# Kernel optimization log

Hardware: AMD Instinct MI355X
Metric: run time of the kernel (lower is better)

The kernel has to match this reference:

```python
import jax, jax.numpy as jnp
import numpy as np

E, D, H = 8, 512, 2048  # num_experts, features, features*mlp_ratio
B, S = 4, 512


def _lecun(key, shape):
    fan_in = shape[-2] if len(shape) >= 2 else shape[0]
    return jax.random.normal(key, shape, dtype=jnp.float32) / jnp.sqrt(jnp.float32(fan_in))


def setup_inputs() -> dict:
    key = jax.random.key(0)
    ks = jax.random.split(key, 8)
    return {
        'x_real': jax.random.normal(ks[0], (B, S, D), dtype=jnp.float32),
        'x_imag': jax.random.normal(ks[1], (B, S, D), dtype=jnp.float32),
        # gating Dense over concat([amp, phase]) -> in_features = 2*D
        'gate_W': _lecun(ks[2], (2 * D, E)),
        'gate_b': jnp.zeros((E,), jnp.float32),
        # per-expert ComplexLinear 1: D -> H
        'W1r': _lecun(ks[3], (E, D, H)),
        'W1i': _lecun(ks[4], (E, D, H)),
        'b1r': jnp.zeros((E, H), jnp.float32),
        'b1i': jnp.zeros((E, H), jnp.float32),
        # per-expert ComplexModReLU bias
        'mod_b': jnp.zeros((E, H), jnp.float32),
        # per-expert ComplexLinear 2: H -> D
        'W2r': _lecun(ks[5], (E, H, D)),
        'W2i': _lecun(ks[6], (E, H, D)),
        'b2r': jnp.zeros((E, D), jnp.float32),
        'b2i': jnp.zeros((E, D), jnp.float32),
    }


def reference(x_real, x_imag, gate_W, gate_b, W1r, W1i, b1r, b1i, mod_b, W2r, W2i, b2r, b2i):
    eps = 1e-10
    # --- gating: scores over [|z|, angle(z)] ---
    amp = jnp.sqrt(x_real ** 2 + x_imag ** 2)            # |z|, [B,S,D]
    phase = jnp.arctan2(x_imag, x_real)                  # angle(z)
    routing_input = jnp.concatenate([amp, phase], axis=-1)  # [B,S,2D]
    scores = routing_input @ gate_W + gate_b             # [B,S,E]
    probs = jax.nn.softmax(scores, axis=-1)
    idx = jnp.argmax(probs, axis=-1)                     # [B,S] top-1 expert

    # --- all experts dense (faithful to reference): complex linear 1 ---
    # (Wr + iWi)(xr + ixi) : hr = xr Wr - xi Wi ; hi = xr Wi + xi Wr
    h_r = (jnp.einsum('bsd,edh->ebsh', x_real, W1r)
           - jnp.einsum('bsd,edh->ebsh', x_imag, W1i)) + b1r[:, None, None, :]
    h_i = (jnp.einsum('bsd,edh->ebsh', x_real, W1i)
           + jnp.einsum('bsd,edh->ebsh', x_imag, W1r)) + b1i[:, None, None, :]

    # --- ComplexModReLU: relu(|z|+b) * z / (|z|+eps), |z| = sqrt(r^2+i^2+eps) ---
    a = jnp.sqrt(h_r ** 2 + h_i ** 2 + eps)              # [E,B,S,H]
    scale = jax.nn.relu(a + mod_b[:, None, None, :]) / (a + eps)
    h_r = h_r * scale
    h_i = h_i * scale

    # --- complex linear 2 ---
    o_r = (jnp.einsum('ebsh,ehd->ebsd', h_r, W2r)
           - jnp.einsum('ebsh,ehd->ebsd', h_i, W2i)) + b2r[:, None, None, :]
    o_i = (jnp.einsum('ebsh,ehd->ebsd', h_r, W2i)
           + jnp.einsum('ebsh,ehd->ebsd', h_i, W2r)) + b2i[:, None, None, :]

    # --- mask + weight (top-1): out = sum_e out_e * probs[...,e] * (argmax==e) ---
    e_ids = jnp.arange(probs.shape[-1])
    w = jnp.transpose(probs, (2, 0, 1)) * (idx[None, :, :] == e_ids[:, None, None])  # [E,B,S]
    out_r = jnp.einsum('ebs,ebsd->bsd', w, o_r)
    out_i = jnp.einsum('ebs,ebsd->bsd', w, o_i)
    return (out_r, out_i)
```

## Files before the change

kernel.cpp:

```cpp
#include <hip/hip_runtime.h>
#include <math.h>

#define NE 8
#define ND 512
#define NH 2048
#define NT 2048

typedef __attribute__((ext_vector_type(8))) short short8;
typedef __attribute__((ext_vector_type(4))) float f32x4;

#define GLL(g, d) __builtin_amdgcn_global_load_lds( \
    (const __attribute__((address_space(1))) void*)(g), \
    (__attribute__((address_space(3))) void*)(d), 16, 0, 0)

__device__ __forceinline__ unsigned short f2bf(float x) {
    unsigned int u = __builtin_bit_cast(unsigned int, x);
    u += 0x7FFFu + ((u >> 16) & 1u);
    return (unsigned short)(u >> 16);
}

__device__ __forceinline__ short8 lds8(const unsigned short* p) {
    return *(const short8*)p;
}

__global__ __launch_bounds__(256) void gate_kernel(
    const float* __restrict__ xr, const float* __restrict__ xi,
    const float* __restrict__ gW, const float* __restrict__ gb,
    float* __restrict__ gate_w,
    int* __restrict__ counts, int* __restrict__ tok_list)
{
    int t = blockIdx.x;
    int tid = threadIdx.x;
    const float* xrt = xr + (size_t)t * ND;
    const float* xit = xi + (size_t)t * ND;

    float acc[NE] = {0,0,0,0,0,0,0,0};
    for (int r = tid; r < 2 * ND; r += 256) {
        int d = r & (ND - 1);
        float a = xrt[d], b = xit[d];
        float v = (r < ND) ? sqrtf(a * a + b * b) : atan2f(b, a);
        const float4* g = (const float4*)(gW + (size_t)r * NE);
        float4 g0 = g[0], g1 = g[1];
        acc[0] += v * g0.x; acc[1] += v * g0.y; acc[2] += v * g0.z; acc[3] += v * g0.w;
        acc[4] += v * g1.x; acc[5] += v * g1.y; acc[6] += v * g1.z; acc[7] += v * g1.w;
    }
    #pragma unroll
    for (int e = 0; e < NE; e++) {
        for (int off = 32; off > 0; off >>= 1)
            acc[e] += __shfl_down(acc[e], off, 64);
    }
    __shared__ float part[4][NE];
    int wave = tid >> 6, lane = tid & 63;
    if (lane == 0) {
        #pragma unroll
        for (int e = 0; e < NE; e++) part[wave][e] = acc[e];
    }
    __syncthreads();
    if (tid == 0) {
        float s[NE];
        #pragma unroll
        for (int e = 0; e < NE; e++)
            s[e] = part[0][e] + part[1][e] + part[2][e] + part[3][e] + gb[e];
        int amax = 0; float m = s[0];
        #pragma unroll
        for (int e = 1; e < NE; e++) if (s[e] > m) { m = s[e]; amax = e; }
        float denom = 0.f;
        #pragma unroll
        for (int e = 0; e < NE; e++) denom += expf(s[e] - m);
        gate_w[t] = 1.0f / denom;
        int pos = atomicAdd(&counts[amax], 1);
        tok_list[amax * NT + pos] = t;
    }
}

__global__ __launch_bounds__(256) void convx_kernel(
    const float* __restrict__ xr, const float* __restrict__ xi,
    unsigned short* __restrict__ obr, unsigned short* __restrict__ obi)
{
    int i = blockIdx.x * 256 + threadIdx.x;
    float4 vr = ((const float4*)xr)[i];
    float4 vi = ((const float4*)xi)[i];
    ((ushort4*)obr)[i] = make_ushort4(f2bf(vr.x), f2bf(vr.y), f2bf(vr.z), f2bf(vr.w));
    ((ushort4*)obi)[i] = make_ushort4(f2bf(vi.x), f2bf(vi.y), f2bf(vi.z), f2bf(vi.w));
}

__global__ __launch_bounds__(256) void transw_kernel(
    const float* __restrict__ s0, unsigned short* __restrict__ d0,
    const float* __restrict__ s1, unsigned short* __restrict__ d1,
    int R, int C)
{
    __shared__ float tile[64][65];
    int e = blockIdx.z;
    int c0 = blockIdx.x * 64, r0 = blockIdx.y * 64;
    size_t off = (size_t)e * R * C;
    int tid = threadIdx.x;
    #pragma unroll
    for (int p = 0; p < 2; ++p) {
        const float* src = (p ? s1 : s0) + off;
        unsigned short* dst = (p ? d1 : d0) + off;
        if (p) __syncthreads();
        for (int i = 0; i < 16; ++i) {
            int idx = tid + i * 256;
            int r = idx >> 6, c = idx & 63;
            tile[r][c] = src[(size_t)(r0 + r) * C + c0 + c];
        }
        __syncthreads();
        #pragma unroll
        for (int i = 0; i < 4; ++i) {
            int c = i * 16 + (tid >> 4);
            int r4 = (tid & 15) * 4;
            ushort4 v = make_ushort4(f2bf(tile[r4][c]), f2bf(tile[r4 + 1][c]),
                                     f2bf(tile[r4 + 2][c]), f2bf(tile[r4 + 3][c]));
            *(ushort4*)&dst[(size_t)(c0 + c) * R + r0 + r4] = v;
        }
    }
}


#define STAGE_(SA_R, SA_I, SB_R, SB_I, ko) do {  \
    GLL(gAr0 + (ko), SA_R + (w * 16) * 64);      \
    GLL(gAi0 + (ko), SA_I + (w * 16) * 64);      \
    GLL(gAr1 + (ko), SA_R + (w * 16 + 8) * 64);  \
    GLL(gAi1 + (ko), SA_I + (w * 16 + 8) * 64);  \
    GLL(gBr0 + (ko), SB_R + (w * 16) * 64);      \
    GLL(gBr1 + (ko), SB_R + (w * 16 + 8) * 64);  \
    GLL(gBi0 + (ko), SB_I + (w * 16) * 64);      \
    GLL(gBi1 + (ko), SB_I + (w * 16 + 8) * 64);  \
} while (0)

#define COMPUTE_(SA_R, SA_I, SB_R, SB_I) do {                                          \
    _Pragma("unroll")                                                                  \
    for (int ks = 0; ks < 2; ++ks) {                                                   \
        int pa = ((ks * 4 + quad) ^ (l15 & 7)) * 8;                                    \
        short8 br  = lds8(SB_R + (w * 16 + l15) * 64 + pa);                            \
        short8 bi2 = lds8(SB_I + (w * 16 + l15) * 64 + pa);                            \
        _Pragma("unroll")                                                              \
        for (int m = 0; m < 4; ++m) {                                                  \
            short8 ar  = lds8(SA_R + (m * 16 + l15) * 64 + pa);                        \
            short8 ai2 = lds8(SA_I + (m * 16 + l15) * 64 + pa);                        \
            aRR[m] = __builtin_amdgcn_mfma_f32_16x16x32_bf16(ar,  br,  aRR[m], 0, 0, 0); \
            aII[m] = __builtin_amdgcn_mfma_f32_16x16x32_bf16(ai2, bi2, aII[m], 0, 0, 0); \
            aRI[m] = __builtin_amdgcn_mfma_f32_16x16x32_bf16(ar,  bi2, aRI[m], 0, 0, 0); \
            aIR[m] = __builtin_amdgcn_mfma_f32_16x16x32_bf16(ai2, br,  aIR[m], 0, 0, 0); \
        }                                                                              \
    }                                                                                  \
} while (0)

#define VMW8  asm volatile("s_waitcnt vmcnt(8)" ::: "memory")
#define VMW0  asm volatile("s_waitcnt vmcnt(0)" ::: "memory")
#define BARX do {                            \
    __builtin_amdgcn_sched_barrier(0);       \
    __builtin_amdgcn_s_barrier();            \
    __builtin_amdgcn_sched_barrier(0);       \
} while (0)

#define MOE_LDS_DECL                                                        \
    __shared__ alignas(16) unsigned short sAr0[4096], sAi0[4096];           \
    __shared__ alignas(16) unsigned short sBr0[4096], sBi0[4096];           \
    __shared__ alignas(16) unsigned short sAr1[4096], sAi1[4096];           \
    __shared__ alignas(16) unsigned short sBr1[4096], sBi1[4096];

#define PIPE_LOOP(NK) do {                                                  \
    STAGE_(sAr0, sAi0, sBr0, sBi0, 0);                                      \
    VMW0; BARX;                                                             \
    _Pragma("unroll 1")                                                     \
    for (int kt = 0; kt < (NK); kt += 2) {                                  \
        if (kt + 1 < (NK)) { STAGE_(sAr1, sAi1, sBr1, sBi1, (kt + 1) * 64); VMW8; } \
        else VMW0;                                                          \
        BARX;                                                               \
        COMPUTE_(sAr0, sAi0, sBr0, sBi0);                                   \
        BARX;                                                               \
        if (kt + 2 < (NK)) { STAGE_(sAr0, sAi0, sBr0, sBi0, (kt + 2) * 64); VMW8; } \
        else VMW0;                                                          \
        BARX;                                                               \
        COMPUTE_(sAr1, sAi1, sBr1, sBi1);                                   \
        BARX;                                                               \
    }                                                                       \
} while (0)

__global__ __launch_bounds__(256, 2) void moe1_kernel(
    const unsigned short* __restrict__ xbr, const unsigned short* __restrict__ xbi,
    const unsigned short* __restrict__ w1tr, const unsigned short* __restrict__ w1ti,
    const float* __restrict__ b1r, const float* __restrict__ b1i,
    const float* __restrict__ mod_b,
    const int* __restrict__ counts, const int* __restrict__ tok_list,
    unsigned short* __restrict__ hr, unsigned short* __restrict__ hi)
{
    int e = blockIdx.z;
    int n = counts[e];
    int mbase = blockIdx.y * 64;
    if (mbase >= n) return;
    int n0 = blockIdx.x * 64;
    int tid = threadIdx.x;
    int w = tid >> 6, l = tid & 63;
    int l15 = l & 15, quad = l >> 4;

    MOE_LDS_DECL

    const int* tl = tok_list + e * NT;
    int swz = (((l & 7) ^ ((l >> 3) & 7)) * 8);
    int ia0 = mbase + w * 16 + (l >> 3);
    int ia1 = ia0 + 8;
    int ra0 = tl[ia0 < n ? ia0 : n - 1];
    int ra1 = tl[ia1 < n ? ia1 : n - 1];
    const unsigned short* gAr0 = xbr + (size_t)ra0 * ND + swz;
    const unsigned short* gAi0 = xbi + (size_t)ra0 * ND + swz;
    const unsigned short* gAr1 = xbr + (size_t)ra1 * ND + swz;
    const unsigned short* gAi1 = xbi + (size_t)ra1 * ND + swz;
    size_t brow = (size_t)e * NH + n0 + w * 16 + (l >> 3);
    const unsigned short* gBr0 = w1tr + brow * ND + swz;
    const unsigned short* gBr1 = w1tr + (brow + 8) * ND + swz;
    const unsigned short* gBi0 = w1ti + brow * ND + swz;
    const unsigned short* gBi1 = w1ti + (brow + 8) * ND + swz;

    f32x4 aRR[4] = {}, aII[4] = {}, aRI[4] = {}, aIR[4] = {};

    PIPE_LOOP(ND / 64);

    int col = n0 + w * 16 + l15;
    float bre = b1r[(size_t)e * NH + col];
    float bie = b1i[(size_t)e * NH + col];
    float mbv = mod_b[(size_t)e * NH + col];
    #pragma unroll
    for (int m = 0; m < 4; ++m) {
        #pragma unroll
        for (int r = 0; r < 4; ++r) {
            int tix = m * 16 + quad * 4 + r;
            if (mbase + tix >= n) continue;
            int tok = tl[mbase + tix];
            float vr = aRR[m][r] - aII[m][r] + bre;
            float vi = aRI[m][r] + aIR[m][r] + bie;
            float a = sqrtf(vr * vr + vi * vi + 1e-10f);
            float sc = fmaxf(a + mbv, 0.0f) / (a + 1e-10f);
            hr[(size_t)tok * NH + col] = f2bf(vr * sc);
            hi[(size_t)tok * NH + col] = f2bf(vi * sc);
        }
    }
}

__global__ __launch_bounds__(256, 2) void moe2_kernel(
    const unsigned short* __restrict__ hr, const unsigned short* __restrict__ hi,
    const unsigned short* __restrict__ w2tr, const unsigned short* __restrict__ w2ti,
    const float* __restrict__ b2r, const float* __restrict__ b2i,
    const int* __restrict__ counts, const int* __restrict__ tok_list,
    const float* __restrict__ gate_w,
    float* __restrict__ out)
{
    int e = blockIdx.z >> 1;
    int ksl = blockIdx.z & 1;
    int n = counts[e];
    int mbase = blockIdx.y * 64;
    if (mbase >= n) return;
    int n0 = blockIdx.x * 64;
    int kbase = ksl * (NH / 2);
    int tid = threadIdx.x;
    int w = tid >> 6, l = tid & 63;
    int l15 = l & 15, quad = l >> 4;

    MOE_LDS_DECL

    const int* tl = tok_list + e * NT;
    int swz = (((l & 7) ^ ((l >> 3) & 7)) * 8);
    int ia0 = mbase + w * 16 + (l >> 3);
    int ia1 = ia0 + 8;
    int ra0 = tl[ia0 < n ? ia0 : n - 1];
    int ra1 = tl[ia1 < n ? ia1 : n - 1];
    const unsigned short* gAr0 = hr + (size_t)ra0 * NH + kbase + swz;
    const unsigned short* gAi0 = hi + (size_t)ra0 * NH + kbase + swz;
    const unsigned short* gAr1 = hr + (size_t)ra1 * NH + kbase + swz;
    const unsigned short* gAi1 = hi + (size_t)ra1 * NH + kbase + swz;
    size_t brow = (size_t)e * ND + n0 + w * 16 + (l >> 3);
    const unsigned short* gBr0 = w2tr + brow * NH + kbase + swz;
    const unsigned short* gBr1 = w2tr + (brow + 8) * NH + kbase + swz;
    const unsigned short* gBi0 = w2ti + brow * NH + kbase + swz;
    const unsigned short* gBi1 = w2ti + (brow + 8) * NH + kbase + swz;

    f32x4 aRR[4] = {}, aII[4] = {}, aRI[4] = {}, aIR[4] = {};

    PIPE_LOOP((NH / 2) / 64);

    int col = n0 + w * 16 + l15;
    float bre = (ksl == 0) ? b2r[(size_t)e * ND + col] : 0.0f;
    float bie = (ksl == 0) ? b2i[(size_t)e * ND + col] : 0.0f;
    #pragma unroll
    for (int m = 0; m < 4; ++m) {
        #pragma unroll
        for (int r = 0; r < 4; ++r) {
            int tix = m * 16 + quad * 4 + r;
            if (mbase + tix >= n) continue;
            int tok = tl[mbase + tix];
            float gw = gate_w[tok];
            atomicAdd(&out[(size_t)tok * ND + col], (aRR[m][r] - aII[m][r] + bre) * gw);
            atomicAdd(&out[(size_t)NT * ND + (size_t)tok * ND + col], (aRI[m][r] + aIR[m][r] + bie) * gw);
        }
    }
}

extern "C" void kernel_launch(void* const* d_in, const int* in_sizes, int n_in,
                              void* d_out, int out_size, void* d_ws, size_t ws_size,
                              hipStream_t stream) {
    const float* xr   = (const float*)d_in[0];
    const float* xi   = (const float*)d_in[1];
    const float* gW   = (const float*)d_in[2];
    const float* gb   = (const float*)d_in[3];
    const float* W1r  = (const float*)d_in[4];
    const float* W1i  = (const float*)d_in[5];
    const float* b1r  = (const float*)d_in[6];
    const float* b1i  = (const float*)d_in[7];
    const float* modb = (const float*)d_in[8];
    const float* W2r  = (const float*)d_in[9];
    const float* W2i  = (const float*)d_in[10];
    const float* b2r  = (const float*)d_in[11];
    const float* b2i  = (const float*)d_in[12];
    float* out = (float*)d_out;

    char* ws = (char*)d_ws;
    int*   counts   = (int*)ws;
    float* gate_w   = (float*)(ws + 256);
    int*   tok_list = (int*)(ws + 256 + 8192);
    size_t off = 256 + 8192 + (size_t)NE * NT * 4;
    unsigned short* xbr  = (unsigned short*)(ws + off); off += (size_t)NT * ND * 2;
    unsigned short* xbi  = (unsigned short*)(ws + off); off += (size_t)NT * ND * 2;
    unsigned short* w1tr = (unsigned short*)(ws + off); off += (size_t)NE * ND * NH * 2;
    unsigned short* w1ti = (unsigned short*)(ws + off); off += (size_t)NE * ND * NH * 2;
    unsigned short* w2tr = (unsigned short*)(ws + off); off += (size_t)NE * ND * NH * 2;
    unsigned short* w2ti = (unsigned short*)(ws + off); off += (size_t)NE * ND * NH * 2;
    unsigned short* h_r  = (unsigned short*)(ws + off); off += (size_t)NT * NH * 2;
    unsigned short* h_i  = (unsigned short*)(ws + off); off += (size_t)NT * NH * 2;

    hipMemsetAsync(counts, 0, 64 * sizeof(int), stream);
    hipMemsetAsync(out, 0, (size_t)out_size * sizeof(float), stream);
    gate_kernel<<<NT, 256, 0, stream>>>(xr, xi, gW, gb, gate_w, counts, tok_list);
    convx_kernel<<<(NT * ND / 4) / 256, 256, 0, stream>>>(xr, xi, xbr, xbi);
    transw_kernel<<<dim3(NH / 64, ND / 64, NE), 256, 0, stream>>>(W1r, w1tr, W1i, w1ti, ND, NH);
    transw_kernel<<<dim3(ND / 64, NH / 64, NE), 256, 0, stream>>>(W2r, w2tr, W2i, w2ti, NH, ND);
    moe1_kernel<<<dim3(NH / 64, NT / 64, NE), 256, 0, stream>>>(
        xbr, xbi, w1tr, w1ti, b1r, b1i, modb, counts, tok_list, h_r, h_i);
    moe2_kernel<<<dim3(ND / 64, NT / 64, NE * 2), 256, 0, stream>>>(
        h_r, h_i, w2tr, w2ti, b2r, b2i, counts, tok_list, gate_w, out);
}
```

Measured before the change: 319.0 us.

## Use persistent work-queue scheduling, register-resident B operands, and fused complex accumulators

Adds a scheduler kernel that builds a compact list of non-empty (expert, M-tile) items. The MoE GEMM kernels become persistent blocks that pull work units from an atomic queue, so no blocks are launched only to exit early. B weight fragments are now loaded straight from global memory into registers, which removes the B LDS staging and halves shared-memory use; occupancy is raised to 3 blocks per SIMD. Complex accumulation folds into two accumulators by negating the imaginary A operand, and moe2 splits K into four slices instead of two. The costs are uncoalesced direct B loads, one atomic per tile, and more output atomics in moe2.

```diff
diff --git a/kernel.cpp b/kernel.cpp
--- a/kernel.cpp
+++ b/kernel.cpp
@@ -17,6 +17,12 @@
     unsigned int u = __builtin_bit_cast(unsigned int, x);
     u += 0x7FFFu + ((u >> 16) & 1u);
     return (unsigned short)(u >> 16);
+}
+
+__device__ __forceinline__ short8 neg8(short8 v) {
+    int4 u = __builtin_bit_cast(int4, v);
+    u.x ^= 0x80008000; u.y ^= 0x80008000; u.z ^= 0x80008000; u.w ^= 0x80008000;
+    return __builtin_bit_cast(short8, u);
 }
 
 __device__ __forceinline__ short8 lds8(const unsigned short* p) {
@@ -70,6 +76,20 @@
         gate_w[t] = 1.0f / denom;
         int pos = atomicAdd(&counts[amax], 1);
         tok_list[amax * NT + pos] = t;
+    }
+}
+
+__global__ void sched_kernel(const int* __restrict__ counts,
+                             int* __restrict__ items, int* __restrict__ nitems)
+{
+    if (threadIdx.x == 0) {
+        int k = 0;
+        for (int e = 0; e < NE; e++) {
+            int n = counts[e];
+            int mt = (n + 63) >> 6;
+            for (int m = 0; m < mt; m++) items[k++] = (e << 16) | m;
+        }
+        nitems[0] = k;
     }
 }
 
@@ -117,31 +137,35 @@
 }
 
 
-#define STAGE_(SA_R, SA_I, SB_R, SB_I, ko) do {  \
+#define STAGEA_(SA_R, SA_I, ko) do {             \
     GLL(gAr0 + (ko), SA_R + (w * 16) * 64);      \
     GLL(gAi0 + (ko), SA_I + (w * 16) * 64);      \
     GLL(gAr1 + (ko), SA_R + (w * 16 + 8) * 64);  \
     GLL(gAi1 + (ko), SA_I + (w * 16 + 8) * 64);  \
-    GLL(gBr0 + (ko), SB_R + (w * 16) * 64);      \
-    GLL(gBr1 + (ko), SB_R + (w * 16 + 8) * 64);  \
-    GLL(gBi0 + (ko), SB_I + (w * 16) * 64);      \
-    GLL(gBi1 + (ko), SB_I + (w * 16 + 8) * 64);  \
-} while (0)
-
-#define COMPUTE_(SA_R, SA_I, SB_R, SB_I) do {                                          \
+} while (0)
+
+#define LOADB_(r0, i0, r1, i1, kt) do {                      \
+    r0 = *(const short8*)(gBr + (size_t)(kt) * 64);          \
+    r1 = *(const short8*)(gBr + (size_t)(kt) * 64 + 32);     \
+    i0 = *(const short8*)(gBi + (size_t)(kt) * 64);          \
+    i1 = *(const short8*)(gBi + (size_t)(kt) * 64 + 32);     \
+} while (0)
+
+#define COMPUTE_(SA_R, SA_I, br0, bi0, br1, bi1) do {                                  \
     _Pragma("unroll")                                                                  \
     for (int ks = 0; ks < 2; ++ks) {                                                   \
         int pa = ((ks * 4 + quad) ^ (l15 & 7)) * 8;                                    \
-        short8 br  = lds8(SB_R + (w * 16 + l15) * 64 + pa);                            \
-        short8 bi2 = lds8(SB_I + (w * 16 + l15) * 64 + pa);                            \
+        short8 br = ks ? br1 : br0;                                                    \
+        short8 bi = ks ? bi1 : bi0;                                                    \
         _Pragma("unroll")                                                              \
         for (int m = 0; m < 4; ++m) {                                                  \
-            short8 ar  = lds8(SA_R + (m * 16 + l15) * 64 + pa);                        \
-            short8 ai2 = lds8(SA_I + (m * 16 + l15) * 64 + pa);                        \
-            aRR[m] = __builtin_amdgcn_mfma_f32_16x16x32_bf16(ar,  br,  aRR[m], 0, 0, 0); \
-            aII[m] = __builtin_amdgcn_mfma_f32_16x16x32_bf16(ai2, bi2, aII[m], 0, 0, 0); \
-            aRI[m] = __builtin_amdgcn_mfma_f32_16x16x32_bf16(ar,  bi2, aRI[m], 0, 0, 0); \
-            aIR[m] = __builtin_amdgcn_mfma_f32_16x16x32_bf16(ai2, br,  aIR[m], 0, 0, 0); \
+            short8 ar = lds8(SA_R + (m * 16 + l15) * 64 + pa);                         \
+            short8 ai = lds8(SA_I + (m * 16 + l15) * 64 + pa);                         \
+            short8 an = neg8(ai);                                                      \
+            accr[m] = __builtin_amdgcn_mfma_f32_16x16x32_bf16(ar, br, accr[m], 0, 0, 0); \
+            accr[m] = __builtin_amdgcn_mfma_f32_16x16x32_bf16(an, bi, accr[m], 0, 0, 0); \
+            acci[m] = __builtin_amdgcn_mfma_f32_16x16x32_bf16(ar, bi, acci[m], 0, 0, 0); \
+            acci[m] = __builtin_amdgcn_mfma_f32_16x16x32_bf16(ai, br, acci[m], 0, 0, 0); \
         }                                                                              \
     }                                                                                  \
 } while (0)
@@ -154,144 +178,172 @@
     __builtin_amdgcn_sched_barrier(0);       \
 } while (0)
 
+#define PIPE8 do {                                                          \
+    STAGEA_(sAr0, sAi0, 0);                                                 \
+    LOADB_(b0r0, b0i0, b0r1, b0i1, 0);                                      \
+    VMW0; BARX;                                                             \
+    _Pragma("unroll 1")                                                     \
+    for (int kt = 0; kt < 8; kt += 2) {                                     \
+        if (kt + 1 < 8) {                                                   \
+            STAGEA_(sAr1, sAi1, (kt + 1) * 64);                             \
+            LOADB_(b1r0, b1i0, b1r1, b1i1, kt + 1);                         \
+            VMW8;                                                           \
+        } else VMW0;                                                        \
+        BARX;                                                               \
+        COMPUTE_(sAr0, sAi0, b0r0, b0i0, b0r1, b0i1);                       \
+        BARX;                                                               \
+        if (kt + 2 < 8) {                                                   \
+            STAGEA_(sAr0, sAi0, (kt + 2) * 64);                             \
+            LOADB_(b0r0, b0i0, b0r1, b0i1, kt + 2);                         \
+            VMW8;                                                           \
+        } else VMW0;                                                        \
+        BARX;                                                               \
+        COMPUTE_(sAr1, sAi1, b1r0, b1i0, b1r1, b1i1);                       \
+        BARX;                                                               \
+    }                                                                       \
+} while (0)
+
 #define MOE_LDS_DECL                                                        \
     __shared__ alignas(16) unsigned short sAr0[4096], sAi0[4096];           \
-    __shared__ alignas(16) unsigned short sBr0[4096], sBi0[4096];           \
     __shared__ alignas(16) unsigned short sAr1[4096], sAi1[4096];           \
-    __shared__ alignas(16) unsigned short sBr1[4096], sBi1[4096];
-
-#define PIPE_LOOP(NK) do {                                                  \
-    STAGE_(sAr0, sAi0, sBr0, sBi0, 0);                                      \
-    VMW0; BARX;                                                             \
-    _Pragma("unroll 1")                                                     \
-    for (int kt = 0; kt < (NK); kt += 2) {                                  \
-        if (kt + 1 < (NK)) { STAGE_(sAr1, sAi1, sBr1, sBi1, (kt + 1) * 64); VMW8; } \
-        else VMW0;                                                          \
-        BARX;                                                               \
-        COMPUTE_(sAr0, sAi0, sBr0, sBi0);                                   \
-        BARX;                                                               \
-        if (kt + 2 < (NK)) { STAGE_(sAr0, sAi0, sBr0, sBi0, (kt + 2) * 64); VMW8; } \
-        else VMW0;                                                          \
-        BARX;                                                               \
-        COMPUTE_(sAr1, sAi1, sBr1, sBi1);                                   \
-        BARX;                                                               \
-    }                                                                       \
-} while (0)
-
-__global__ __launch_bounds__(256, 2) void moe1_kernel(
+    __shared__ int s_u;
+
+__global__ __launch_bounds__(256, 3) void moe1_kernel(
     const unsigned short* __restrict__ xbr, const unsigned short* __restrict__ xbi,
     const unsigned short* __restrict__ w1tr, const unsigned short* __restrict__ w1ti,
     const float* __restrict__ b1r, const float* __restrict__ b1i,
     const float* __restrict__ mod_b,
     const int* __restrict__ counts, const int* __restrict__ tok_list,
+    const int* __restrict__ items, const int* __restrict__ nitems,
+    int* __restrict__ q,
     unsigned short* __restrict__ hr, unsigned short* __restrict__ hi)
 {
-    int e = blockIdx.z;
-    int n = counts[e];
-    int mbase = blockIdx.y * 64;
-    if (mbase >= n) return;
-    int n0 = blockIdx.x * 64;
     int tid = threadIdx.x;
     int w = tid >> 6, l = tid & 63;
     int l15 = l & 15, quad = l >> 4;
+    int swz = (((l & 7) ^ ((l >> 3) & 7)) * 8);
 
     MOE_LDS_DECL
 
-    const int* tl = tok_list + e * NT;
-    int swz = (((l & 7) ^ ((l >> 3) & 7)) * 8);
-    int ia0 = mbase + w * 16 + (l >> 3);
-    int ia1 = ia0 + 8;
-    int ra0 = tl[ia0 < n ? ia0 : n - 1];
-    int ra1 = tl[ia1 < n ? ia1 : n - 1];
-    const unsigned short* gAr0 = xbr + (size_t)ra0 * ND + swz;
-    const unsigned short* gAi0 = xbi + (size_t)ra0 * ND + swz;
-    const unsigned short* gAr1 = xbr + (size_t)ra1 * ND + swz;
-    const unsigned short* gAi1 = xbi + (size_t)ra1 * ND + swz;
-    size_t brow = (size_t)e * NH + n0 + w * 16 + (l >> 3);
-    const unsigned short* gBr0 = w1tr + brow * ND + swz;
-    const unsigned short* gBr1 = w1tr + (brow + 8) * ND + swz;
-    const unsigned short* gBi0 = w1ti + brow * ND + swz;
-    const unsigned short* gBi1 = w1ti + (brow + 8) * ND + swz;
-
-    f32x4 aRR[4] = {}, aII[4] = {}, aRI[4] = {}, aIR[4] = {};
-
-    PIPE_LOOP(ND / 64);
-
-    int col = n0 + w * 16 + l15;
-    float bre = b1r[(size_t)e * NH + col];
-    float bie = b1i[(size_t)e * NH + col];
-    float mbv = mod_b[(size_t)e * NH + col];
-    #pragma unroll
-    for (int m = 0; m < 4; ++m) {
-        #pragma unroll
-        for (int r = 0; r < 4; ++r) {
-            int tix = m * 16 + quad * 4 + r;
-            if (mbase + tix >= n) continue;
-            int tok = tl[mbase + tix];
-            float vr = aRR[m][r] - aII[m][r] + bre;
-            float vi = aRI[m][r] + aIR[m][r] + bie;
-            float a = sqrtf(vr * vr + vi * vi + 1e-10f);
-            float sc = fmaxf(a + mbv, 0.0f) / (a + 1e-10f);
-            hr[(size_t)tok * NH + col] = f2bf(vr * sc);
-            hi[(size_t)tok * NH + col] = f2bf(vi * sc);
-        }
-    }
-}
-
-__global__ __launch_bounds__(256, 2) void moe2_kernel(
+    int total = nitems[0] * 32;
+
+    for (;;) {
+        __syncthreads();
+        if (tid == 0) s_u = atomicAdd(q, 1);
+        __syncthreads();
+        int u = s_u;
+        if (u >= total) return;
+
+        int it = items[u >> 5];
+        int nt = u & 31;
+        int e = it >> 16, mt = it & 0xffff;
+        int n = counts[e];
+        int mbase = mt * 64, n0 = nt * 64;
+        const int* tl = tok_list + e * NT;
+
+        int ia0 = mbase + w * 16 + (l >> 3);
+        int ia1 = ia0 + 8;
+        int ra0 = tl[ia0 < n ? ia0 : n - 1];
+        int ra1 = tl[ia1 < n ? ia1 : n - 1];
+        const unsigned short* gAr0 = xbr + (size_t)ra0 * ND + swz;
+        const unsigned short* gAi0 = xbi + (size_t)ra0 * ND + swz;
+        const unsigned short* gAr1 = xbr + (size_t)ra1 * ND + swz;
+        const unsigned short* gAi1 = xbi + (size_t)ra1 * ND + swz;
+        const unsigned short* gBr = w1tr + ((size_t)e * NH + n0 + w * 16 + l15) * ND + quad * 8;
+        const unsigned short* gBi = w1ti + ((size_t)e * NH + n0 + w * 16 + l15) * ND + quad * 8;
+
+        f32x4 accr[4] = {}, acci[4] = {};
+        short8 b0r0, b0i0, b0r1, b0i1, b1r0, b1i0, b1r1, b1i1;
+
+        PIPE8;
+
+        int col = n0 + w * 16 + l15;
+        float bre = b1r[(size_t)e * NH + col];
+        float bie = b1i[(size_t)e * NH + col];
+        float mbv = mod_b[(size_t)e * NH + col];
+        #pragma unroll
+        for (int m = 0; m < 4; ++m) {
+            #pragma unroll
+            for (int r = 0; r < 4; ++r) {
+                int tix = m * 16 + quad * 4 + r;
+                if (mbase + tix >= n) continue;
+                int tok = tl[mbase + tix];
+                float vr = accr[m][r] + bre;
+                float vi = acci[m][r] + bie;
+                float a = sqrtf(vr * vr + vi * vi + 1e-10f);
+                float sc = fmaxf(a + mbv, 0.0f) / (a + 1e-10f);
+                hr[(size_t)tok * NH + col] = f2bf(vr * sc);
+                hi[(size_t)tok * NH + col] = f2bf(vi * sc);
+            }
+        }
+    }
+}
+
+__global__ __launch_bounds__(256, 3) void moe2_kernel(
     const unsigned short* __restrict__ hr, const unsigned short* __restrict__ hi,
     const unsigned short* __restrict__ w2tr, const unsigned short* __restrict__ w2ti,
     const float* __restrict__ b2r, const float* __restrict__ b2i,
     const int* __restrict__ counts, const int* __restrict__ tok_list,
+    const int* __restrict__ items, const int* __restrict__ nitems,
+    int* __restrict__ q,
     const float* __restrict__ gate_w,
     float* __restrict__ out)
 {
-    int e = blockIdx.z >> 1;
-    int ksl = blockIdx.z & 1;
-    int n = counts[e];
-    int mbase = blockIdx.y * 64;
-    if (mbase >= n) return;
-    int n0 = blockIdx.x * 64;
-    int kbase = ksl * (NH / 2);
     int tid = threadIdx.x;
     int w = tid >> 6, l = tid & 63;
     int l15 = l & 15, quad = l >> 4;
+    int swz = (((l & 7) ^ ((l >> 3) & 7)) * 8);
 
     MOE_LDS_DECL
 
-    const int* tl = tok_list + e * NT;
-    int swz = (((l & 7) ^ ((l >> 3) & 7)) * 8);
-    int ia0 = mbase + w * 16 + (l >> 3);
-    int ia1 = ia0 + 8;
-    int ra0 = tl[ia0 < n ? ia0 : n - 1];
-    int ra1 = tl[ia1 < n ? ia1 : n - 1];
-    const unsigned short* gAr0 = hr + (size_t)ra0 * NH + kbase + swz;
-    const unsigned short* gAi0 = hi + (size_t)ra0 * NH + kbase + swz;
-    const unsigned short* gAr1 = hr + (size_t)ra1 * NH + kbase + swz;
-    const unsigned short* gAi1 = hi + (size_t)ra1 * NH + kbase + swz;
-    size_t brow = (size_t)e * ND + n0 + w * 16 + (l >> 3);
-    const unsigned short* gBr0 = w2tr + brow * NH + kbase + swz;
-    const unsigned short* gBr1 = w2tr + (brow + 8) * NH + kbase + swz;
-    const unsigned short* gBi0 = w2ti + brow * NH + kbase + swz;
-    const unsigned short* gBi1 = w2ti + (brow + 8) * NH + kbase + swz;
-
-    f32x4 aRR[4] = {}, aII[4] = {}, aRI[4] = {}, aIR[4] = {};
-
-    PIPE_LOOP((NH / 2) / 64);
-
-    int col = n0 + w * 16 + l15;
-    float bre = (ksl == 0) ? b2r[(size_t)e * ND + col] : 0.0f;
-    float bie = (ksl == 0) ? b2i[(size_t)e * ND + col] : 0.0f;
-    #pragma unroll
-    for (int m = 0; m < 4; ++m) {
-        #pragma unroll
-        for (int r = 0; r < 4; ++r) {
-            int tix = m * 16 + quad * 4 + r;
-            if (mbase + tix >= n) continue;
-            int tok = tl[mbase + tix];
-            float gw = gate_w[tok];
-            atomicAdd(&out[(size_t)tok * ND + col], (aRR[m][r] - aII[m][r] + bre) * gw);
-            atomicAdd(&out[(size_t)NT * ND + (size_t)tok * ND + col], (aRI[m][r] + aIR[m][r] + bie) * gw);
+    int total = nitems[0] * 32;
+
+    for (;;) {
+        __syncthreads();
+        if (tid == 0) s_u = atomicAdd(q, 1);
+        __syncthreads();
+        int u = s_u;
+        if (u >= total) return;
+
+        int it = items[u >> 5];
+        int nt = u & 7;
+        int ksl = (u >> 3) & 3;
+        int e = it >> 16, mt = it & 0xffff;
+        int n = counts[e];
+        int mbase = mt * 64, n0 = nt * 64;
+        int kbase = ksl * (NH / 4);
+        const int* tl = tok_list + e * NT;
+
+        int ia0 = mbase + w * 16 + (l >> 3);
+        int ia1 = ia0 + 8;
+        int ra0 = tl[ia0 < n ? ia0 : n - 1];
+        int ra1 = tl[ia1 < n ? ia1 : n - 1];
+        const unsigned short* gAr0 = hr + (size_t)ra0 * NH + kbase + swz;
+        const unsigned short* gAi0 = hi + (size_t)ra0 * NH + kbase + swz;
+        const unsigned short* gAr1 = hr + (size_t)ra1 * NH + kbase + swz;
+        const unsigned short* gAi1 = hi + (size_t)ra1 * NH + kbase + swz;
+        const unsigned short* gBr = w2tr + ((size_t)e * ND + n0 + w * 16 + l15) * NH + kbase + quad * 8;
+        const unsigned short* gBi = w2ti + ((size_t)e * ND + n0 + w * 16 + l15) * NH + kbase + quad * 8;
+
+        f32x4 accr[4] = {}, acci[4] = {};
+        short8 b0r0, b0i0, b0r1, b0i1, b1r0, b1i0, b1r1, b1i1;
+
+        PIPE8;
+
+        int col = n0 + w * 16 + l15;
+        float bre = (ksl == 0) ? b2r[(size_t)e * ND + col] : 0.0f;
+        float bie = (ksl == 0) ? b2i[(size_t)e * ND + col] : 0.0f;
+        #pragma unroll
+        for (int m = 0; m < 4; ++m) {
+            #pragma unroll
+            for (int r = 0; r < 4; ++r) {
+                int tix = m * 16 + quad * 4 + r;
+                if (mbase + tix >= n) continue;
+                int tok = tl[mbase + tix];
+                float gw = gate_w[tok];
+                atomicAdd(&out[(size_t)tok * ND + col], (accr[m][r] + bre) * gw);
+                atomicAdd(&out[(size_t)NT * ND + (size_t)tok * ND + col], (acci[m][r] + bie) * gw);
+            }
         }
     }
 }
@@ -319,6 +371,8 @@
     float* gate_w   = (float*)(ws + 256);
     int*   tok_list = (int*)(ws + 256 + 8192);
     size_t off = 256 + 8192 + (size_t)NE * NT * 4;
+    int*   items    = (int*)(ws + off); off += 256;
+    int*   nitems   = (int*)(ws + off); off += 256;
     unsigned short* xbr  = (unsigned short*)(ws + off); off += (size_t)NT * ND * 2;
     unsigned short* xbi  = (unsigned short*)(ws + off); off += (size_t)NT * ND * 2;
     unsigned short* w1tr = (unsigned short*)(ws + off); off += (size_t)NE * ND * NH * 2;
@@ -328,14 +382,18 @@
     unsigned short* h_r  = (unsigned short*)(ws + off); off += (size_t)NT * NH * 2;
     unsigned short* h_i  = (unsigned short*)(ws + off); off += (size_t)NT * NH * 2;
 
+    int* q1 = counts + 8;
+    int* q2 = counts + 9;
+
     hipMemsetAsync(counts, 0, 64 * sizeof(int), stream);
     hipMemsetAsync(out, 0, (size_t)out_size * sizeof(float), stream);
     gate_kernel<<<NT, 256, 0, stream>>>(xr, xi, gW, gb, gate_w, counts, tok_list);
+    sched_kernel<<<1, 64, 0, stream>>>(counts, items, nitems);
     convx_kernel<<<(NT * ND / 4) / 256, 256, 0, stream>>>(xr, xi, xbr, xbi);
     transw_kernel<<<dim3(NH / 64, ND / 64, NE), 256, 0, stream>>>(W1r, w1tr, W1i, w1ti, ND, NH);
     transw_kernel<<<dim3(ND / 64, NH / 64, NE), 256, 0, stream>>>(W2r, w2tr, W2i, w2ti, NH, ND);
-    moe1_kernel<<<dim3(NH / 64, NT / 64, NE), 256, 0, stream>>>(
-        xbr, xbi, w1tr, w1ti, b1r, b1i, modb, counts, tok_list, h_r, h_i);
-    moe2_kernel<<<dim3(ND / 64, NT / 64, NE * 2), 256, 0, stream>>>(
-        h_r, h_i, w2tr, w2ti, b2r, b2i, counts, tok_list, gate_w, out);
-}
+    moe1_kernel<<<768, 256, 0, stream>>>(
+        xbr, xbi, w1tr, w1ti, b1r, b1i, modb, counts, tok_list, items, nitems, q1, h_r, h_i);
+    moe2_kernel<<<768, 256, 0, stream>>>(
+        h_r, h_i, w2tr, w2ti, b2r, b2i, counts, tok_list, items, nitems, q2, gate_w, out);
+}
```

After: 349.6 us. +9.6%, slower.

## Use persistent work-list scheduling for MoE GEMMs and drop split-K atomics

Applied to the files above, without the earlier changes.

Adds a tiny scheduling kernel that builds a compact list of (expert, m-tile) items from the per-expert counts. The two MoE GEMM kernels become persistent 512-block kernels that each walk a contiguous chunk of tiles, so no empty blocks are launched. The second GEMM now runs the full K range per tile and writes the output directly instead of using split-K atomicAdd, which removes the output memset. The bf16 conversion of x is folded into the gate kernel, removing a separate launch. The costs are an extra serial scheduling launch, less parallelism in the second GEMM, and load imbalance from static chunking.

```diff
diff --git a/kernel.cpp b/kernel.cpp
--- a/kernel.cpp
+++ b/kernel.cpp
@@ -27,12 +27,19 @@
     const float* __restrict__ xr, const float* __restrict__ xi,
     const float* __restrict__ gW, const float* __restrict__ gb,
     float* __restrict__ gate_w,
-    int* __restrict__ counts, int* __restrict__ tok_list)
+    int* __restrict__ counts, int* __restrict__ tok_list,
+    unsigned short* __restrict__ obr, unsigned short* __restrict__ obi)
 {
     int t = blockIdx.x;
     int tid = threadIdx.x;
     const float* xrt = xr + (size_t)t * ND;
     const float* xit = xi + (size_t)t * ND;
+
+    #pragma unroll
+    for (int d = tid; d < ND; d += 256) {
+        obr[(size_t)t * ND + d] = f2bf(xrt[d]);
+        obi[(size_t)t * ND + d] = f2bf(xit[d]);
+    }
 
     float acc[NE] = {0,0,0,0,0,0,0,0};
     for (int r = tid; r < 2 * ND; r += 256) {
@@ -73,15 +80,18 @@
     }
 }
 
-__global__ __launch_bounds__(256) void convx_kernel(
-    const float* __restrict__ xr, const float* __restrict__ xi,
-    unsigned short* __restrict__ obr, unsigned short* __restrict__ obi)
-{
-    int i = blockIdx.x * 256 + threadIdx.x;
-    float4 vr = ((const float4*)xr)[i];
-    float4 vi = ((const float4*)xi)[i];
-    ((ushort4*)obr)[i] = make_ushort4(f2bf(vr.x), f2bf(vr.y), f2bf(vr.z), f2bf(vr.w));
-    ((ushort4*)obi)[i] = make_ushort4(f2bf(vi.x), f2bf(vi.y), f2bf(vi.z), f2bf(vi.w));
+__global__ void sched_kernel(const int* __restrict__ counts,
+                             int* __restrict__ items, int* __restrict__ nitems)
+{
+    if (threadIdx.x == 0) {
+        int k = 0;
+        for (int e = 0; e < NE; e++) {
+            int n = counts[e];
+            int mt = (n + 63) >> 6;
+            for (int m = 0; m < mt; m++) items[k++] = (e << 16) | m;
+        }
+        nitems[0] = k;
+    }
 }
 
 __global__ __launch_bounds__(256) void transw_kernel(
@@ -178,62 +188,73 @@
     }                                                                       \
 } while (0)
 
+#define NBLK 512
+
 __global__ __launch_bounds__(256, 2) void moe1_kernel(
     const unsigned short* __restrict__ xbr, const unsigned short* __restrict__ xbi,
     const unsigned short* __restrict__ w1tr, const unsigned short* __restrict__ w1ti,
     const float* __restrict__ b1r, const float* __restrict__ b1i,
     const float* __restrict__ mod_b,
     const int* __restrict__ counts, const int* __restrict__ tok_list,
+    const int* __restrict__ items, const int* __restrict__ nitems,
     unsigned short* __restrict__ hr, unsigned short* __restrict__ hi)
 {
-    int e = blockIdx.z;
-    int n = counts[e];
-    int mbase = blockIdx.y * 64;
-    if (mbase >= n) return;
-    int n0 = blockIdx.x * 64;
     int tid = threadIdx.x;
     int w = tid >> 6, l = tid & 63;
     int l15 = l & 15, quad = l >> 4;
+    int swz = (((l & 7) ^ ((l >> 3) & 7)) * 8);
 
     MOE_LDS_DECL
 
-    const int* tl = tok_list + e * NT;
-    int swz = (((l & 7) ^ ((l >> 3) & 7)) * 8);
-    int ia0 = mbase + w * 16 + (l >> 3);
-    int ia1 = ia0 + 8;
-    int ra0 = tl[ia0 < n ? ia0 : n - 1];
-    int ra1 = tl[ia1 < n ? ia1 : n - 1];
-    const unsigned short* gAr0 = xbr + (size_t)ra0 * ND + swz;
-    const unsigned short* gAi0 = xbi + (size_t)ra0 * ND + swz;
-    const unsigned short* gAr1 = xbr + (size_t)ra1 * ND + swz;
-    const unsigned short* gAi1 = xbi + (size_t)ra1 * ND + swz;
-    size_t brow = (size_t)e * NH + n0 + w * 16 + (l >> 3);
-    const unsigned short* gBr0 = w1tr + brow * ND + swz;
-    const unsigned short* gBr1 = w1tr + (brow + 8) * ND + swz;
-    const unsigned short* gBi0 = w1ti + brow * ND + swz;
-    const unsigned short* gBi1 = w1ti + (brow + 8) * ND + swz;
-
-    f32x4 aRR[4] = {}, aII[4] = {}, aRI[4] = {}, aIR[4] = {};
-
-    PIPE_LOOP(ND / 64);
-
-    int col = n0 + w * 16 + l15;
-    float bre = b1r[(size_t)e * NH + col];
-    float bie = b1i[(size_t)e * NH + col];
-    float mbv = mod_b[(size_t)e * NH + col];
-    #pragma unroll
-    for (int m = 0; m < 4; ++m) {
-        #pragma unroll
-        for (int r = 0; r < 4; ++r) {
-            int tix = m * 16 + quad * 4 + r;
-            if (mbase + tix >= n) continue;
-            int tok = tl[mbase + tix];
-            float vr = aRR[m][r] - aII[m][r] + bre;
-            float vi = aRI[m][r] + aIR[m][r] + bie;
-            float a = sqrtf(vr * vr + vi * vi + 1e-10f);
-            float sc = fmaxf(a + mbv, 0.0f) / (a + 1e-10f);
-            hr[(size_t)tok * NH + col] = f2bf(vr * sc);
-            hi[(size_t)tok * NH + col] = f2bf(vi * sc);
+    int total = nitems[0] * 32;
+    int chunk = (total + NBLK - 1) / NBLK;
+    int u0 = blockIdx.x * chunk;
+    int u1 = u0 + chunk; if (u1 > total) u1 = total;
+
+    for (int u = u0; u < u1; ++u) {
+        int it = items[u >> 5];
+        int nt = u & 31;
+        int e = it >> 16, mt = it & 0xffff;
+        int n = counts[e];
+        int mbase = mt * 64, n0 = nt * 64;
+        const int* tl = tok_list + e * NT;
+
+        int ia0 = mbase + w * 16 + (l >> 3);
+        int ia1 = ia0 + 8;
+        int ra0 = tl[ia0 < n ? ia0 : n - 1];
+        int ra1 = tl[ia1 < n ? ia1 : n - 1];
+        const unsigned short* gAr0 = xbr + (size_t)ra0 * ND + swz;
+        const unsigned short* gAi0 = xbi + (size_t)ra0 * ND + swz;
+        const unsigned short* gAr1 = xbr + (size_t)ra1 * ND + swz;
+        const unsigned short* gAi1 = xbi + (size_t)ra1 * ND + swz;
+        size_t brow = (size_t)e * NH + n0 + w * 16 + (l >> 3);
+        const unsigned short* gBr0 = w1tr + brow * ND + swz;
+        const unsigned short* gBr1 = w1tr + (brow + 8) * ND + swz;
+        const unsigned short* gBi0 = w1ti + brow * ND + swz;
+        const unsigned short* gBi1 = w1ti + (brow + 8) * ND + swz;
+
+        f32x4 aRR[4] = {}, aII[4] = {}, aRI[4] = {}, aIR[4] = {};
+
+        PIPE_LOOP(ND / 64);
+
+        int col = n0 + w * 16 + l15;
+        float bre = b1r[(size_t)e * NH + col];
+        float bie = b1i[(size_t)e * NH + col];
+        float mbv = mod_b[(size_t)e * NH + col];
+        #pragma unroll
+        for (int m = 0; m < 4; ++m) {
+            #pragma unroll
+            for (int r = 0; r < 4; ++r) {
+                int tix = m * 16 + quad * 4 + r;
+                if (mbase + tix >= n) continue;
+                int tok = tl[mbase + tix];
+                float vr = aRR[m][r] - aII[m][r] + bre;
+                float vi = aRI[m][r] + aIR[m][r] + bie;
+                float a = sqrtf(vr * vr + vi * vi + 1e-10f);
+                float sc = fmaxf(a + mbv, 0.0f) / (a + 1e-10f);
+                hr[(size_t)tok * NH + col] = f2bf(vr * sc);
+                hi[(size_t)tok * NH + col] = f2bf(vi * sc);
+            }
         }
     }
 }
@@ -243,55 +264,62 @@
     const unsigned short* __restrict__ w2tr, const unsigned short* __restrict__ w2ti,
     const float* __restrict__ b2r, const float* __restrict__ b2i,
     const int* __restrict__ counts, const int* __restrict__ tok_list,
+    const int* __restrict__ items, const int* __restrict__ nitems,
     const float* __restrict__ gate_w,
     float* __restrict__ out)
 {
-    int e = blockIdx.z >> 1;
-    int ksl = blockIdx.z & 1;
-    int n = counts[e];
-    int mbase = blockIdx.y * 64;
-    if (mbase >= n) return;
-    int n0 = blockIdx.x * 64;
-    int kbase = ksl * (NH / 2);
     int tid = threadIdx.x;
     int w = tid >> 6, l = tid & 63;
     int l15 = l & 15, quad = l >> 4;
+    int swz = (((l & 7) ^ ((l >> 3) & 7)) * 8);
 
     MOE_LDS_DECL
 
-    const int* tl = tok_list + e * NT;
-    int swz = (((l & 7) ^ ((l >> 3) & 7)) * 8);
-    int ia0 = mbase + w * 16 + (l >> 3);
-    int ia1 = ia0 + 8;
-    int ra0 = tl[ia0 < n ? ia0 : n - 1];
-    int ra1 = tl[ia1 < n ? ia1 : n - 1];
-    const unsigned short* gAr0 = hr + (size_t)ra0 * NH + kbase + swz;
-    const unsigned short* gAi0 = hi + (size_t)ra0 * NH + kbase + swz;
-    const unsigned short* gAr1 = hr + (size_t)ra1 * NH + kbase + swz;
-    const unsigned short* gAi1 = hi + (size_t)ra1 * NH + kbase + swz;
-    size_t brow = (size_t)e * ND + n0 + w * 16 + (l >> 3);
-    const unsigned short* gBr0 = w2tr + brow * NH + kbase + swz;
-    const unsigned short* gBr1 = w2tr + (brow + 8) * NH + kbase + swz;
-    const unsigned short* gBi0 = w2ti + brow * NH + kbase + swz;
-    const unsigned short* gBi1 = w2ti + (brow + 8) * NH + kbase + swz;
-
-    f32x4 aRR[4] = {}, aII[4] = {}, aRI[4] = {}, aIR[4] = {};
-
-    PIPE_LOOP((NH / 2) / 64);
-
-    int col = n0 + w * 16 + l15;
-    float bre = (ksl == 0) ? b2r[(size_t)e * ND + col] : 0.0f;
-    float bie = (ksl == 0) ? b2i[(size_t)e * ND + col] : 0.0f;
-    #pragma unroll
-    for (int m = 0; m < 4; ++m) {
-        #pragma unroll
-        for (int r = 0; r < 4; ++r) {
-            int tix = m * 16 + quad * 4 + r;
-            if (mbase + tix >= n) continue;
-            int tok = tl[mbase + tix];
-            float gw = gate_w[tok];
-            atomicAdd(&out[(size_t)tok * ND + col], (aRR[m][r] - aII[m][r] + bre) * gw);
-            atomicAdd(&out[(size_t)NT * ND + (size_t)tok * ND + col], (aRI[m][r] + aIR[m][r] + bie) * gw);
+    int total = nitems[0] * 8;
+    int chunk = (total + NBLK - 1) / NBLK;
+    int u0 = blockIdx.x * chunk;
+    int u1 = u0 + chunk; if (u1 > total) u1 = total;
+
+    for (int u = u0; u < u1; ++u) {
+        int it = items[u >> 3];
+        int nt = u & 7;
+        int e = it >> 16, mt = it & 0xffff;
+        int n = counts[e];
+        int mbase = mt * 64, n0 = nt * 64;
+        const int* tl = tok_list + e * NT;
+
+        int ia0 = mbase + w * 16 + (l >> 3);
+        int ia1 = ia0 + 8;
+        int ra0 = tl[ia0 < n ? ia0 : n - 1];
+        int ra1 = tl[ia1 < n ? ia1 : n - 1];
+        const unsigned short* gAr0 = hr + (size_t)ra0 * NH + swz;
+        const unsigned short* gAi0 = hi + (size_t)ra0 * NH + swz;
+        const unsigned short* gAr1 = hr + (size_t)ra1 * NH + swz;
+        const unsigned short* gAi1 = hi + (size_t)ra1 * NH + swz;
+        size_t brow = (size_t)e * ND + n0 + w * 16 + (l >> 3);
+        const unsigned short* gBr0 = w2tr + brow * NH + swz;
+        const unsigned short* gBr1 = w2tr + (brow + 8) * NH + swz;
+        const unsigned short* gBi0 = w2ti + brow * NH + swz;
+        const unsigned short* gBi1 = w2ti + (brow + 8) * NH + swz;
+
+        f32x4 aRR[4] = {}, aII[4] = {}, aRI[4] = {}, aIR[4] = {};
+
+        PIPE_LOOP(NH / 64);
+
+        int col = n0 + w * 16 + l15;
+        float bre = b2r[(size_t)e * ND + col];
+        float bie = b2i[(size_t)e * ND + col];
+        #pragma unroll
+        for (int m = 0; m < 4; ++m) {
+            #pragma unroll
+            for (int r = 0; r < 4; ++r) {
+                int tix = m * 16 + quad * 4 + r;
+                if (mbase + tix >= n) continue;
+                int tok = tl[mbase + tix];
+                float gw = gate_w[tok];
+                out[(size_t)tok * ND + col] = (aRR[m][r] - aII[m][r] + bre) * gw;
+                out[(size_t)NT * ND + (size_t)tok * ND + col] = (aRI[m][r] + aIR[m][r] + bie) * gw;
+            }
         }
     }
 }
@@ -319,6 +347,8 @@
     float* gate_w   = (float*)(ws + 256);
     int*   tok_list = (int*)(ws + 256 + 8192);
     size_t off = 256 + 8192 + (size_t)NE * NT * 4;
+    int*   items    = (int*)(ws + off); off += 256;
+    int*   nitems   = (int*)(ws + off); off += 256;
     unsigned short* xbr  = (unsigned short*)(ws + off); off += (size_t)NT * ND * 2;
     unsigned short* xbi  = (unsigned short*)(ws + off); off += (size_t)NT * ND * 2;
     unsigned short* w1tr = (unsigned short*)(ws + off); off += (size_t)NE * ND * NH * 2;
@@ -329,13 +359,12 @@
     unsigned short* h_i  = (unsigned short*)(ws + off); off += (size_t)NT * NH * 2;
 
     hipMemsetAsync(counts, 0, 64 * sizeof(int), stream);
-    hipMemsetAsync(out, 0, (size_t)out_size * sizeof(float), stream);
-    gate_kernel<<<NT, 256, 0, stream>>>(xr, xi, gW, gb, gate_w, counts, tok_list);
-    convx_kernel<<<(NT * ND / 4) / 256, 256, 0, stream>>>(xr, xi, xbr, xbi);
+    gate_kernel<<<NT, 256, 0, stream>>>(xr, xi, gW, gb, gate_w, counts, tok_list, xbr, xbi);
+    sched_kernel<<<1, 64, 0, stream>>>(counts, items, nitems);
     transw_kernel<<<dim3(NH / 64, ND / 64, NE), 256, 0, stream>>>(W1r, w1tr, W1i, w1ti, ND, NH);
     transw_kernel<<<dim3(ND / 64, NH / 64, NE), 256, 0, stream>>>(W2r, w2tr, W2i, w2ti, NH, ND);
-    moe1_kernel<<<dim3(NH / 64, NT / 64, NE), 256, 0, stream>>>(
-        xbr, xbi, w1tr, w1ti, b1r, b1i, modb, counts, tok_list, h_r, h_i);
-    moe2_kernel<<<dim3(ND / 64, NT / 64, NE * 2), 256, 0, stream>>>(
-        h_r, h_i, w2tr, w2ti, b2r, b2i, counts, tok_list, gate_w, out);
-}
+    moe1_kernel<<<NBLK, 256, 0, stream>>>(
+        xbr, xbi, w1tr, w1ti, b1r, b1i, modb, counts, tok_list, items, nitems, h_r, h_i);
+    moe2_kernel<<<NBLK, 256, 0, stream>>>(
+        h_r, h_i, w2tr, w2ti, b2r, b2i, counts, tok_list, items, nitems, gate_w, out);
+}
```

After: 311.3 us. -2.4%, faster.
